# Kernel tuning notes

Hardware: AMD Instinct MI355X
Metric: run time of the kernel (lower is better)

Reference implementation:

```python
import jax, jax.numpy as jnp
import numpy as np

B, S, D, H = 4, 2048, 1024, 16
HD = D // H

def setup_inputs() -> dict:
    key = jax.random.key(0)
    ks = jax.random.split(key, 12)
    std = 1.0 / np.sqrt(D)
    inp = {
        'query': jax.random.normal(ks[0], (B, S, D), jnp.float32),
        'key':   jax.random.normal(ks[1], (B, S, D), jnp.float32),
        'value': jax.random.normal(ks[2], (B, S, D), jnp.float32),
        'mask':  jnp.tril(jnp.ones((S, S), jnp.int32))[None, None, :, :],  # [1,1,S,S] causal
        'Wq': jax.random.uniform(ks[3], (D, D), jnp.float32, -std, std),
        'bq': jax.random.uniform(ks[4], (D,), jnp.float32, -std, std),
        'Wk': jax.random.uniform(ks[5], (D, D), jnp.float32, -std, std),
        'bk': jax.random.uniform(ks[6], (D,), jnp.float32, -std, std),
        'Wv': jax.random.uniform(ks[7], (D, D), jnp.float32, -std, std),
        'bv': jax.random.uniform(ks[8], (D,), jnp.float32, -std, std),
        'Wo': jax.random.uniform(ks[9], (D, D), jnp.float32, -std, std),
        'bo': jax.random.uniform(ks[10], (D,), jnp.float32, -std, std),
    }
    return inp

def _split_heads(x, W, b):
    # torch Linear: x @ W.T + b ; then [B,S,H,HD] -> [B,H,S,HD]
    y = jnp.einsum('bsd,ed->bse', x, W) + b
    return y.reshape(x.shape[0], -1, H, HD).transpose(0, 2, 1, 3)

def reference(query, key, value, mask, Wq, bq, Wk, bk, Wv, bv, Wo, bo):
    q = _split_heads(query, Wq, bq)   # [B,H,S,HD]
    k = _split_heads(key,   Wk, bk)
    v = _split_heads(value, Wv, bv)
    logits = jnp.einsum('bhqd,bhkd->bhqk', q, k) / np.sqrt(HD)  # [B,H,S,S]
    logits = jnp.where(mask == 0, jnp.float32(-1e9), logits)
    attn = jax.nn.softmax(logits, axis=-1)
    out = jnp.einsum('bhqk,bhkd->bhqd', attn, v)               # [B,H,S,HD]
    out = out.transpose(0, 2, 1, 3).reshape(query.shape[0], -1, D)
    return jnp.einsum('bsd,ed->bse', out, Wo) + bo
```

## Files before the change

kernel.cpp:

```cpp
#include <hip/hip_runtime.h>
#include <hip/hip_bf16.h>


#define SLEN 2048
#define DMOD 1024

typedef __attribute__((ext_vector_type(8))) short s16x8;
typedef __attribute__((ext_vector_type(4))) float f32x4;

__device__ __forceinline__ unsigned short f2bf(float f) {
    union { __hip_bfloat16 h; unsigned short u; } cv;
    cv.h = __float2bfloat16(f);
    return cv.u;
}
__device__ __forceinline__ unsigned pack2bf(float a, float b) {
    return (unsigned)f2bf(a) | ((unsigned)f2bf(b) << 16);
}

__device__ __forceinline__ void gload_lds16(const void* g, void* l) {
    __builtin_amdgcn_global_load_lds(
        (const __attribute__((address_space(1))) void*)g,
        (__attribute__((address_space(3))) void*)l, 16, 0, 0);
}

__global__ __launch_bounds__(256) void convert_bf16(
    const float* __restrict__ q, const float* __restrict__ k,
    const float* __restrict__ v, const float* __restrict__ wq,
    const float* __restrict__ wk, const float* __restrict__ wv,
    const float* __restrict__ wo, unsigned short* __restrict__ ws)
{
    const int bid = blockIdx.x, tid = threadIdx.x;
    const float* src;
    unsigned short* dst;
    size_t off;
    if (bid < 3072) {
        const int t = bid >> 10;
        src = (t == 0) ? q : (t == 1) ? k : v;
        dst = ws + (size_t)t * 8388608;
        off = (size_t)(bid & 1023) * 8192;
    } else {
        const int w = (bid - 3072) >> 7;
        src = (w == 0) ? wq : (w == 1) ? wk : (w == 2) ? wv : wo;
        dst = ws + 25165824 + (size_t)w * 1048576;
        off = (size_t)((bid - 3072) & 127) * 8192;
    }
#pragma unroll
    for (int i = 0; i < 8; ++i) {
        const size_t e = off + (size_t)(i * 256 + tid) * 4;
        float4 x = *reinterpret_cast<const float4*>(&src[e]);
        uint2 u;
        u.x = pack2bf(x.x, x.y);
        u.y = pack2bf(x.z, x.w);
        *reinterpret_cast<uint2*>(&dst[e]) = u;
    }
}

template<int MODE>
__global__ __launch_bounds__(256) void gemm_bf16(
    const unsigned short* __restrict__ A, const unsigned short* __restrict__ W,
    const float* __restrict__ bias, void* __restrict__ outp)
{
    __shared__ unsigned short Asm[2][8192];
    __shared__ unsigned short Bsm[2][8192];

    const int tid  = threadIdx.x;
    const int lane = tid & 63, wid = tid >> 6;
    const int l15 = lane & 15, lhi = lane >> 4;

    const int flat = blockIdx.x;
    const int logical = (flat & 7) * 64 + (flat >> 3);
    const int m0 = (logical >> 3) * 128, n0 = (logical & 7) * 128;

    const int wr = wid >> 1, wc = wid & 1;
    const int srow = lane >> 3;
    const int sgr  = (lane & 7) ^ srow;

    int aoff[2][4], boff[2][4];
#pragma unroll
    for (int kk = 0; kk < 2; ++kk)
#pragma unroll
        for (int i = 0; i < 4; ++i) {
            const int s = ((4 * kk + lhi) ^ (l15 & 7)) * 16;
            aoff[kk][i] = (wr * 64 + i * 16 + l15) * 128 + s;
            boff[kk][i] = (wc * 64 + i * 16 + l15) * 128 + s;
        }

    const unsigned short* apt = A + (size_t)(m0 + wid * 8 + srow) * 1024 + sgr * 8;
    const unsigned short* bpt = W + (size_t)(n0 + wid * 8 + srow) * 1024 + sgr * 8;

    f32x4 acc[4][4];
#pragma unroll
    for (int i = 0; i < 4; ++i)
#pragma unroll
        for (int j = 0; j < 4; ++j) acc[i][j] = (f32x4)0.f;

    auto stage = [&](int bsel) {
        char* ad = (char*)Asm + bsel * 16384 + wid * 1024;
        char* bd = (char*)Bsm + bsel * 16384 + wid * 1024;
#pragma unroll
        for (int i = 0; i < 4; ++i) {
            gload_lds16(apt + i * 32768, ad + i * 4096);
            gload_lds16(bpt + i * 32768, bd + i * 4096);
        }
        apt += 64; bpt += 64;
    };

    stage(0);
    __syncthreads();
    int cur = 0;
#pragma unroll 1
    for (int kt = 0; kt < 16; ++kt) {
        if (kt < 15) stage(cur ^ 1);
        const char* AB = (const char*)Asm + cur * 16384;
        const char* BB = (const char*)Bsm + cur * 16384;
#pragma unroll
        for (int kk = 0; kk < 2; ++kk) {
            s16x8 af[4], bfv[4];
#pragma unroll
            for (int i = 0; i < 4; ++i) af[i]  = *reinterpret_cast<const s16x8*>(AB + aoff[kk][i]);
#pragma unroll
            for (int j = 0; j < 4; ++j) bfv[j] = *reinterpret_cast<const s16x8*>(BB + boff[kk][j]);
#pragma unroll
            for (int i = 0; i < 4; ++i)
#pragma unroll
                for (int j = 0; j < 4; ++j)
                    acc[i][j] = __builtin_amdgcn_mfma_f32_16x16x32_bf16(af[i], bfv[j], acc[i][j], 0, 0, 0);
        }
        __syncthreads();
        cur ^= 1;
    }

#pragma unroll
    for (int j = 0; j < 4; ++j) {
        const int col = n0 + wc * 64 + j * 16 + l15;
        const float bv = bias[col];
#pragma unroll
        for (int i = 0; i < 4; ++i) {
#pragma unroll
            for (int r = 0; r < 4; ++r) {
                const int row = m0 + wr * 64 + i * 16 + lhi * 4 + r;
                const float val = acc[i][j][r] + bv;
                if constexpr (MODE == 2) {
                    ((float*)outp)[(size_t)row * 1024 + col] = val;
                } else if constexpr (MODE == 0) {
                    ((unsigned short*)outp)[(size_t)((row >> 11) * 16 + (col >> 6)) * 131072
                                            + (size_t)(row & 2047) * 64 + (col & 63)] = f2bf(val);
                } else {
                    ((unsigned short*)outp)[(size_t)((row >> 11) * 16 + (col >> 6)) * 131072
                                            + (size_t)(col & 63) * 2048 + (row & 2047)] = f2bf(val);
                }
            }
        }
    }
}

#define EXPC 0.18033688011112043f

__global__ __launch_bounds__(256, 4) void attn_kernel(
    const unsigned short* __restrict__ Q,
    const unsigned short* __restrict__ Kc,
    const unsigned short* __restrict__ Vt,
    unsigned short* __restrict__ Ao)
{
    __shared__ unsigned short Kbuf[2][4096];
    __shared__ unsigned short Vbuf[2][4096];
    __shared__ unsigned short Psm[4][1024];

    const int tid = threadIdx.x, lane = tid & 63, wid = tid >> 6;
    const int l15 = lane & 15, lhi = lane >> 4;
    const int sK = l15 & 7;
    const int sub = lane >> 3, c8s = lane & 7;
    const int thr = wid * 16 + l15;

    int ko[8], pr[2], pw[4];
#pragma unroll
    for (int kk = 0; kk < 2; ++kk) {
        pr[kk] = (l15 * 8 + ((4 * kk + lhi) ^ sK)) * 16;
#pragma unroll
        for (int nb = 0; nb < 4; ++nb)
            ko[kk * 4 + nb] = ((nb * 16 + l15) * 8 + ((4 * kk + lhi) ^ sK)) * 16;
    }
#pragma unroll
    for (int nb = 0; nb < 4; ++nb)
        pw[nb] = (l15 * 16 + ((nb * 4 + lhi) ^ (2 * sK))) * 8;

    const int flat = blockIdx.x;
    const int logical = (flat & 7) * 128 + (flat >> 3);
    const int bx = logical & 15, bh = logical >> 4;

    const size_t base = (size_t)bh * SLEN * 64;
    const unsigned short* Qb = Q + base;
    const unsigned short* Kb = Kc + base;
    const unsigned short* Vb = Vt + base;
    const int b = bh >> 4, h = bh & 15;
    const int scol = (c8s ^ sub) * 8;

#pragma unroll 1
    for (int seg = 0; seg < 2; ++seg) {
        const int qt = seg ? (31 - bx) : bx;
        const int q0 = qt * 64;

        s16x8 aq[2];
#pragma unroll
        for (int kk = 0; kk < 2; ++kk)
            aq[kk] = *reinterpret_cast<const s16x8*>(
                &Qb[(size_t)(q0 + wid * 16 + l15) * 64 + kk * 32 + 8 * lhi]);

        f32x4 o_acc[4];
#pragma unroll
        for (int nb = 0; nb < 4; ++nb) o_acc[nb] = (f32x4)0.f;
        float m_r = -1e30f, l_part = 0.f;

        const unsigned short* kpt = Kb + (16 * wid + sub) * 64 + scol;
        const unsigned short* vpt = Vb + (size_t)(16 * wid + sub) * SLEN + scol;

        auto stage = [&](int bsel) {
            char* kd = (char*)Kbuf + bsel * 8192 + wid * 2048;
            char* vd = (char*)Vbuf + bsel * 8192 + wid * 2048;
            gload_lds16(kpt,         kd);
            gload_lds16(kpt + 512,   kd + 1024);
            gload_lds16(vpt,         vd);
            gload_lds16(vpt + 16384, vd + 1024);
            kpt += 4096; vpt += 64;
        };

        auto tile = [&](int cbo, bool domask) {
            const char* KB = (const char*)Kbuf + cbo;
            const char* VB = (const char*)Vbuf + cbo;
            char* PW = (char*)Psm + wid * 2048;

            f32x4 sc2[4];
#pragma unroll
            for (int nb = 0; nb < 4; ++nb) sc2[nb] = (f32x4)0.f;
            __builtin_amdgcn_s_setprio(1);
#pragma unroll
            for (int kk = 0; kk < 2; ++kk) {
                s16x8 ak[4];
#pragma unroll
                for (int nb = 0; nb < 4; ++nb)
                    ak[nb] = *reinterpret_cast<const s16x8*>(KB + ko[kk * 4 + nb]);
#pragma unroll
                for (int nb = 0; nb < 4; ++nb)
                    sc2[nb] = __builtin_amdgcn_mfma_f32_16x16x32_bf16(ak[nb], aq[kk], sc2[nb], 0, 0, 0);
            }
            __builtin_amdgcn_s_setprio(0);

            float tmx = -3e30f;
#pragma unroll
            for (int nb = 0; nb < 4; ++nb)
#pragma unroll
                for (int r = 0; r < 4; ++r) {
                    float x = sc2[nb][r];
                    if (domask && (nb * 16 + lhi * 4 + r > thr)) x = -3e30f;
                    sc2[nb][r] = x;
                    tmx = fmaxf(tmx, x);
                }

            if (__any(tmx - m_r > 64.0f)) {
                float tf = fmaxf(tmx, __shfl_xor(tmx, 16));
                tf = fmaxf(tf, __shfl_xor(tf, 32));
                const float mn = fmaxf(m_r, tf);
                const float alpha = exp2f((m_r - mn) * EXPC);
                m_r = mn;
                l_part *= alpha;
                float ar[4];
#pragma unroll
                for (int r = 0; r < 4; ++r) ar[r] = __shfl(alpha, lhi * 4 + r);
#pragma unroll
                for (int nb = 0; nb < 4; ++nb)
#pragma unroll
                    for (int r = 0; r < 4; ++r) o_acc[nb][r] *= ar[r];
            }

            const float negmC = -m_r * EXPC;
#pragma unroll
            for (int nb = 0; nb < 4; ++nb) {
                float p0 = exp2f(fmaf(sc2[nb][0], EXPC, negmC));
                float p1 = exp2f(fmaf(sc2[nb][1], EXPC, negmC));
                float p2 = exp2f(fmaf(sc2[nb][2], EXPC, negmC));
                float p3 = exp2f(fmaf(sc2[nb][3], EXPC, negmC));
                l_part += (p0 + p1) + (p2 + p3);
                uint2 u;
                u.x = pack2bf(p0, p1);
                u.y = pack2bf(p2, p3);
                *reinterpret_cast<uint2*>(PW + pw[nb]) = u;
            }

            __builtin_amdgcn_s_setprio(1);
#pragma unroll
            for (int kk = 0; kk < 2; ++kk) {
                s16x8 pa = *reinterpret_cast<const s16x8*>(PW + pr[kk]);
                s16x8 bvv[4];
#pragma unroll
                for (int nb = 0; nb < 4; ++nb)
                    bvv[nb] = *reinterpret_cast<const s16x8*>(VB + ko[kk * 4 + nb]);
#pragma unroll
                for (int nb = 0; nb < 4; ++nb)
                    o_acc[nb] = __builtin_amdgcn_mfma_f32_16x16x32_bf16(pa, bvv[nb], o_acc[nb], 0, 0, 0);
            }
            __builtin_amdgcn_s_setprio(0);
        };

        stage(0);
        __syncthreads();
        int cur = 0;

#pragma unroll 1
        for (int t = 0; t < qt; ++t) {
            stage(cur ^ 1);
            tile(cur * 8192, false);
            __syncthreads();
            cur ^= 1;
        }
        tile(cur * 8192, true);

        float lf = l_part + __shfl_xor(l_part, 16);
        lf += __shfl_xor(lf, 32);
        float linv[4];
#pragma unroll
        for (int r = 0; r < 4; ++r)
            linv[r] = 1.0f / __shfl(lf, lhi * 4 + r);
#pragma unroll
        for (int nb = 0; nb < 4; ++nb)
#pragma unroll
            for (int r = 0; r < 4; ++r) {
                const int s = q0 + wid * 16 + lhi * 4 + r;
                Ao[((size_t)b * SLEN + s) * DMOD + h * 64 + nb * 16 + l15] =
                    f2bf(o_acc[nb][r] * linv[r]);
            }
        __syncthreads();
    }
}

extern "C" void kernel_launch(void* const* d_in, const int* in_sizes, int n_in,
                              void* d_out, int out_size, void* d_ws, size_t ws_size,
                              hipStream_t stream) {
    const float* q  = (const float*)d_in[0];
    const float* k  = (const float*)d_in[1];
    const float* v  = (const float*)d_in[2];
    const float* Wq = (const float*)d_in[4];
    const float* bq = (const float*)d_in[5];
    const float* Wk = (const float*)d_in[6];
    const float* bk = (const float*)d_in[7];
    const float* Wv = (const float*)d_in[8];
    const float* bv = (const float*)d_in[9];
    const float* Wo = (const float*)d_in[10];
    const float* bo = (const float*)d_in[11];

    unsigned short* wsp = (unsigned short*)d_ws;
    unsigned short* qc  = wsp;
    unsigned short* kc  = wsp + 8388608;
    unsigned short* vc  = wsp + 16777216;
    unsigned short* wqc = wsp + 25165824;
    unsigned short* wkc = wsp + 26214400;
    unsigned short* wvc = wsp + 27262976;
    unsigned short* woc = wsp + 28311552;
    unsigned short* qb  = wsp + 29360128;
    unsigned short* kb  = wsp + 37748736;
    unsigned short* vtb = wsp + 46137344;
    unsigned short* ao  = qc;

    dim3 gb(256);
    convert_bf16<<<dim3(3584), gb, 0, stream>>>(q, k, v, Wq, Wk, Wv, Wo, wsp);
    gemm_bf16<0><<<dim3(512), gb, 0, stream>>>(qc, wqc, bq, qb);
    gemm_bf16<0><<<dim3(512), gb, 0, stream>>>(kc, wkc, bk, kb);
    gemm_bf16<1><<<dim3(512), gb, 0, stream>>>(vc, wvc, bv, vtb);
    attn_kernel<<<dim3(1024), gb, 0, stream>>>(qb, kb, vtb, ao);
    gemm_bf16<2><<<dim3(512), gb, 0, stream>>>(ao, woc, bo, (float*)d_out);
}
```

Baseline: 190.5 us.

## Compute softmax row sums via MFMA with ones and use packed bf16 convert

Replaces the per-lane scalar accumulation of softmax denominators, along with its final cross-lane shuffles, with an extra MFMA that multiplies the bf16 probability tile by a ones vector. The row sums then land in the same layout as the output accumulator. Scalar bf16 packing is replaced by the hardware v_cvt_pk_bf16_f32 instruction, and the score accumulator zero-init is folded into the first MFMA. The denominator is now summed from bf16-rounded probabilities, which matches the numerator but adds MFMA work per tile.

```diff
diff --git a/kernel.cpp b/kernel.cpp
--- a/kernel.cpp
+++ b/kernel.cpp
@@ -13,8 +13,10 @@
     cv.h = __float2bfloat16(f);
     return cv.u;
 }
-__device__ __forceinline__ unsigned pack2bf(float a, float b) {
-    return (unsigned)f2bf(a) | ((unsigned)f2bf(b) << 16);
+__device__ __forceinline__ unsigned cvtpk(float a, float b) {
+    unsigned r;
+    asm("v_cvt_pk_bf16_f32 %0, %1, %2" : "=v"(r) : "v"(a), "v"(b));
+    return r;
 }
 
 __device__ __forceinline__ void gload_lds16(const void* g, void* l) {
@@ -49,8 +51,8 @@
         const size_t e = off + (size_t)(i * 256 + tid) * 4;
         float4 x = *reinterpret_cast<const float4*>(&src[e]);
         uint2 u;
-        u.x = pack2bf(x.x, x.y);
-        u.y = pack2bf(x.z, x.w);
+        u.x = cvtpk(x.x, x.y);
+        u.y = cvtpk(x.z, x.w);
         *reinterpret_cast<uint2*>(&dst[e]) = u;
     }
 }
@@ -195,6 +197,9 @@
     const int b = bh >> 4, h = bh & 15;
     const int scol = (c8s ^ sub) * 8;
 
+    const f32x4 fzero = (f32x4)0.f;
+    const s16x8 onesb = (s16x8)(short)0x3F80;
+
 #pragma unroll 1
     for (int seg = 0; seg < 2; ++seg) {
         const int qt = seg ? (31 - bx) : bx;
@@ -209,7 +214,8 @@
         f32x4 o_acc[4];
 #pragma unroll
         for (int nb = 0; nb < 4; ++nb) o_acc[nb] = (f32x4)0.f;
-        float m_r = -1e30f, l_part = 0.f;
+        f32x4 l_acc = (f32x4)0.f;
+        float m_r = -1e30f;
 
         const unsigned short* kpt = Kb + (16 * wid + sub) * 64 + scol;
         const unsigned short* vpt = Vb + (size_t)(16 * wid + sub) * SLEN + scol;
@@ -230,8 +236,6 @@
             char* PW = (char*)Psm + wid * 2048;
 
             f32x4 sc2[4];
-#pragma unroll
-            for (int nb = 0; nb < 4; ++nb) sc2[nb] = (f32x4)0.f;
             __builtin_amdgcn_s_setprio(1);
 #pragma unroll
             for (int kk = 0; kk < 2; ++kk) {
@@ -241,20 +245,24 @@
                     ak[nb] = *reinterpret_cast<const s16x8*>(KB + ko[kk * 4 + nb]);
 #pragma unroll
                 for (int nb = 0; nb < 4; ++nb)
-                    sc2[nb] = __builtin_amdgcn_mfma_f32_16x16x32_bf16(ak[nb], aq[kk], sc2[nb], 0, 0, 0);
+                    sc2[nb] = __builtin_amdgcn_mfma_f32_16x16x32_bf16(
+                        ak[nb], aq[kk], kk == 0 ? fzero : sc2[nb], 0, 0, 0);
             }
             __builtin_amdgcn_s_setprio(0);
 
-            float tmx = -3e30f;
+            if (domask) {
+#pragma unroll
+                for (int nb = 0; nb < 4; ++nb)
+#pragma unroll
+                    for (int r = 0; r < 4; ++r)
+                        if (nb * 16 + lhi * 4 + r > thr) sc2[nb][r] = -3e30f;
+            }
+            float tm[4];
 #pragma unroll
             for (int nb = 0; nb < 4; ++nb)
-#pragma unroll
-                for (int r = 0; r < 4; ++r) {
-                    float x = sc2[nb][r];
-                    if (domask && (nb * 16 + lhi * 4 + r > thr)) x = -3e30f;
-                    sc2[nb][r] = x;
-                    tmx = fmaxf(tmx, x);
-                }
+                tm[nb] = fmaxf(fmaxf(sc2[nb][0], sc2[nb][1]),
+                               fmaxf(sc2[nb][2], sc2[nb][3]));
+            float tmx = fmaxf(fmaxf(tm[0], tm[1]), fmaxf(tm[2], tm[3]));
 
             if (__any(tmx - m_r > 64.0f)) {
                 float tf = fmaxf(tmx, __shfl_xor(tmx, 16));
@@ -262,10 +270,11 @@
                 const float mn = fmaxf(m_r, tf);
                 const float alpha = exp2f((m_r - mn) * EXPC);
                 m_r = mn;
-                l_part *= alpha;
                 float ar[4];
 #pragma unroll
                 for (int r = 0; r < 4; ++r) ar[r] = __shfl(alpha, lhi * 4 + r);
+#pragma unroll
+                for (int r = 0; r < 4; ++r) l_acc[r] *= ar[r];
 #pragma unroll
                 for (int nb = 0; nb < 4; ++nb)
 #pragma unroll
@@ -279,10 +288,9 @@
                 float p1 = exp2f(fmaf(sc2[nb][1], EXPC, negmC));
                 float p2 = exp2f(fmaf(sc2[nb][2], EXPC, negmC));
                 float p3 = exp2f(fmaf(sc2[nb][3], EXPC, negmC));
-                l_part += (p0 + p1) + (p2 + p3);
                 uint2 u;
-                u.x = pack2bf(p0, p1);
-                u.y = pack2bf(p2, p3);
+                u.x = cvtpk(p0, p1);
+                u.y = cvtpk(p2, p3);
                 *reinterpret_cast<uint2*>(PW + pw[nb]) = u;
             }
 
@@ -297,6 +305,7 @@
 #pragma unroll
                 for (int nb = 0; nb < 4; ++nb)
                     o_acc[nb] = __builtin_amdgcn_mfma_f32_16x16x32_bf16(pa, bvv[nb], o_acc[nb], 0, 0, 0);
+                l_acc = __builtin_amdgcn_mfma_f32_16x16x32_bf16(pa, onesb, l_acc, 0, 0, 0);
             }
             __builtin_amdgcn_s_setprio(0);
         };
@@ -314,12 +323,9 @@
         }
         tile(cur * 8192, true);
 
-        float lf = l_part + __shfl_xor(l_part, 16);
-        lf += __shfl_xor(lf, 32);
         float linv[4];
 #pragma unroll
-        for (int r = 0; r < 4; ++r)
-            linv[r] = 1.0f / __shfl(lf, lhi * 4 + r);
+        for (int r = 0; r < 4; ++r) linv[r] = 1.0f / l_acc[r];
 #pragma unroll
         for (int nb = 0; nb < 4; ++nb)
 #pragma unroll
```

Result: no change. 188.0 us (-1.3%).
